# Kernel tuning notes

Measured on AMD Instinct MI355X. Metric: run time of the kernel, lower is better.

The kernel has to match this reference:

```python
import jax, jax.numpy as jnp
import numpy as np

B, D = 4096, 1024

def setup_inputs() -> dict:
    key = jax.random.key(0)
    k1, k2, k3 = jax.random.split(key, 3)
    # q, p are row-stochastic probability distributions (original calls q.log())
    q = jax.nn.softmax(jax.random.normal(k1, (B, D), dtype=jnp.float32), axis=-1)
    p = jax.nn.softmax(jax.random.normal(k2, (B, D), dtype=jnp.float32), axis=-1)
    # binary same-class indicator matrix
    labels_matrix = jax.random.randint(k3, (B, B), 0, 2).astype(jnp.float32)
    return {"q": q, "p": p, "labels_matrix": labels_matrix}

def reference(q, p, labels_matrix):
    d = q.shape[1]
    log_q = jnp.log(q)
    log_p = jnp.log(p)
    # torch kl_div(log_q, p) = p * (log p - log q); mean over feature dim -> [B]
    kl_div = jnp.mean(p * (log_p - log_q), axis=1)
    # pairwise kl_dis[i, j] = mean_d p[j,d] * (log p[j,d] - log q[i,d])
    # = (sum_d p[j] log p[j] - (log_q @ p^T)[i, j]) / D  -- single GEMM, no BxBxD tensor
    p_entropy_term = jnp.sum(p * log_p, axis=1)          # [B]
    cross = log_q @ p.T                                   # [B, B]
    kl_dis = (p_entropy_term[None, :] - cross) / d        # [B, B]
    # original detaches kl_dis via .cpu().numpy()
    kl_dis = jax.lax.stop_gradient(kl_dis)
    positive = kl_div + jnp.sum(kl_dis * labels_matrix, axis=1)
    negative = jnp.sum(kl_dis * (1.0 - labels_matrix), axis=1)
    return jnp.sum(positive / negative)
```

## Files before the change

kernel.cpp:

```cpp
#include <hip/hip_runtime.h>
#include <hip/hip_bf16.h>
#include <stdint.h>

#define BROWS 4096
#define DDIM  1024
#define LSTR  72

typedef float f32x4 __attribute__((ext_vector_type(4)));
#define PSCALE 64.0f
#define INV_PSCALE 0.015625f

__device__ __forceinline__ int pack4_fp8(float a, float b, float c, float d) {
    int w = __builtin_amdgcn_cvt_pk_fp8_f32(a, b, 0, false);
    w = __builtin_amdgcn_cvt_pk_fp8_f32(c, d, w, true);
    return w;
}

__global__ __launch_bounds__(256) void prep_kernel(
    const float* __restrict__ q, const float* __restrict__ p,
    const float* __restrict__ L,
    int* __restrict__ lq8, int* __restrict__ p8,
    uint64_t* __restrict__ Lb,
    float* __restrict__ e, float* __restrict__ kld,
    float* __restrict__ CS, float* __restrict__ CL, float* __restrict__ EL)
{
    const int row = blockIdx.x;
    const int t   = threadIdx.x;
    const int wv  = t >> 6, ln = t & 63;

    const float4* qv4 = (const float4*)(q + (size_t)row * DDIM);
    const float4* pv4 = (const float4*)(p + (size_t)row * DDIM);
    float4 qv = qv4[t];
    float4 pv = pv4[t];

    float lq0 = __logf(qv.x), lq1 = __logf(qv.y), lq2 = __logf(qv.z), lq3 = __logf(qv.w);
    float lp0 = __logf(pv.x), lp1 = __logf(pv.y), lp2 = __logf(pv.z), lp3 = __logf(pv.w);

    float esum = pv.x * lp0 + pv.y * lp1 + pv.z * lp2 + pv.w * lp3;
    float ksum = pv.x * (lp0 - lq0) + pv.y * (lp1 - lq1)
               + pv.z * (lp2 - lq2) + pv.w * (lp3 - lq3);

    lq8[row * 256 + t] = pack4_fp8(lq0, lq1, lq2, lq3);
    p8 [row * 256 + t] = pack4_fp8(pv.x * PSCALE, pv.y * PSCALE,
                                   pv.z * PSCALE, pv.w * PSCALE);

    const float* Lrow = L + (size_t)row * BROWS;
    #pragma unroll
    for (int c = 0; c < 16; c++) {
        float v = Lrow[c * 256 + t];
        unsigned long long m = __ballot(v != 0.0f);
        if (ln == 0) Lb[(size_t)row * 64 + c * 4 + wv] = m;
    }

    if (t == 0) { CS[row] = 0.f; CL[row] = 0.f; EL[row] = 0.f; }

    #pragma unroll
    for (int off = 32; off > 0; off >>= 1) {
        esum += __shfl_down(esum, off);
        ksum += __shfl_down(ksum, off);
    }
    __shared__ float se[4], sk[4];
    if (ln == 0) { se[wv] = esum; sk[wv] = ksum; }
    __syncthreads();
    if (t == 0) {
        e[row]   = se[0] + se[1] + se[2] + se[3];
        kld[row] = (sk[0] + sk[1] + sk[2] + sk[3]) * (1.0f / DDIM);
    }
}

__global__ __launch_bounds__(1024, 4) void gemm_epi_kernel(
    const uint8_t* __restrict__ A8,
    const uint8_t* __restrict__ B8,
    const uint64_t* __restrict__ Lb,
    const float*  __restrict__ e,
    float* __restrict__ CS, float* __restrict__ CL, float* __restrict__ EL)
{
    __shared__ __align__(16) uint8_t As[256 * LSTR];
    __shared__ __align__(16) uint8_t Bs[256 * LSTR];

    const int t    = threadIdx.x;
    const int i0   = blockIdx.y * 256;
    const int j0   = blockIdx.x * 256;
    const int wave = t >> 6;
    const int lane = t & 63;
    const int q4   = lane >> 4;
    const int ln   = lane & 15;
    const int wrow = wave & 3;
    const int wcol = wave >> 2;

    f32x4 acc[4][4];
    #pragma unroll
    for (int a = 0; a < 4; a++)
        #pragma unroll
        for (int b = 0; b < 4; b++)
            acc[a][b] = (f32x4){0.f, 0.f, 0.f, 0.f};

    const int srow = t >> 2;
    const int scol = (t & 3) * 16;
    const uint8_t* gA = A8 + (size_t)(i0 + srow) * DDIM + scol;
    const uint8_t* gB = B8 + (size_t)(j0 + srow) * DDIM + scol;
    const int loff = srow * LSTR + scol;

    int4 pfA[2], pfB[2];
    pfA[0] = *(const int4*)(gA);       pfB[0] = *(const int4*)(gB);
    pfA[1] = *(const int4*)(gA + 64);  pfB[1] = *(const int4*)(gB + 64);

    #pragma unroll 1
    for (int c = 0; c < DDIM / 64; ++c) {
        const int buf = c & 1;
        __syncthreads();
        *(int4*)(As + loff) = pfA[buf];
        *(int4*)(Bs + loff) = pfB[buf];
        __syncthreads();

        if (c + 2 < DDIM / 64) {
            pfA[buf] = *(const int4*)(gA + (c + 2) * 64);
            pfB[buf] = *(const int4*)(gB + (c + 2) * 64);
        }

        #pragma unroll
        for (int ks = 0; ks < 2; ks++) {
            long af[4], bfv[4];
            #pragma unroll
            for (int mi = 0; mi < 4; mi++)
                af[mi] = *(const long*)(As + (wrow * 64 + mi * 16 + ln) * LSTR
                                           + ks * 32 + q4 * 8);
            #pragma unroll
            for (int ni = 0; ni < 4; ni++)
                bfv[ni] = *(const long*)(Bs + (wcol * 64 + ni * 16 + ln) * LSTR
                                            + ks * 32 + q4 * 8);
            #pragma unroll
            for (int mi = 0; mi < 4; mi++)
                #pragma unroll
                for (int ni = 0; ni < 4; ni++)
                    acc[mi][ni] = __builtin_amdgcn_mfma_f32_16x16x32_fp8_fp8(
                        af[mi], bfv[ni], acc[mi][ni], 0, 0, 0);
        }
    }

    const int i_base = i0 + wrow * 64;
    const int j_base = j0 + wcol * 64;

    float e_j[4];
    #pragma unroll
    for (int ni = 0; ni < 4; ni++) e_j[ni] = e[j_base + ni * 16 + ln];

    #pragma unroll
    for (int mi = 0; mi < 4; mi++) {
        #pragma unroll
        for (int r = 0; r < 4; r++) {
            const int i = i_base + mi * 16 + q4 * 4 + r;
            const uint64_t m  = Lb[(size_t)i * 64 + (j_base >> 6)];
            const uint64_t ms = m >> ln;
            float cs = 0.f, cl = 0.f, el = 0.f;
            #pragma unroll
            for (int ni = 0; ni < 4; ni++) {
                float c = acc[mi][ni][r];
                cs += c;
                if ((ms >> (ni * 16)) & 1ull) { cl += c; el += e_j[ni]; }
            }
            #pragma unroll
            for (int s = 1; s < 16; s <<= 1) {
                cs += __shfl_xor(cs, s);
                cl += __shfl_xor(cl, s);
                el += __shfl_xor(el, s);
            }
            if (ln == 0) {
                atomicAdd(&CS[i], cs * INV_PSCALE);
                atomicAdd(&CL[i], cl * INV_PSCALE);
                atomicAdd(&EL[i], el);
            }
        }
    }
}

__global__ __launch_bounds__(1024) void final_kernel(
    const float* __restrict__ e, const float* __restrict__ kld,
    const float* __restrict__ CS, const float* __restrict__ CL,
    const float* __restrict__ EL, float* __restrict__ out)
{
    __shared__ float sred[16];
    __shared__ float sEtot;
    const int t = threadIdx.x;
    const int wv = t >> 6, ln = t & 63;

    float s = 0.f;
    for (int j = t; j < BROWS; j += 1024) s += e[j];
    #pragma unroll
    for (int off = 32; off > 0; off >>= 1) s += __shfl_down(s, off);
    if (ln == 0) sred[wv] = s;
    __syncthreads();
    if (t == 0) {
        float a = 0.f;
        #pragma unroll
        for (int k = 0; k < 16; k++) a += sred[k];
        sEtot = a;
    }
    __syncthreads();
    const float Etot = sEtot;
    const float invD = 1.0f / DDIM;

    float rs = 0.f;
    for (int i = t; i < BROWS; i += 1024) {
        float el = EL[i], cl = CL[i], cs = CS[i];
        float pos = kld[i] + (el - cl) * invD;
        float neg = (Etot - el - cs + cl) * invD;
        rs += pos / neg;
    }
    __syncthreads();
    #pragma unroll
    for (int off = 32; off > 0; off >>= 1) rs += __shfl_down(rs, off);
    if (ln == 0) sred[wv] = rs;
    __syncthreads();
    if (t == 0) {
        float a = 0.f;
        #pragma unroll
        for (int k = 0; k < 16; k++) a += sred[k];
        out[0] = a;
    }
}

extern "C" void kernel_launch(void* const* d_in, const int* in_sizes, int n_in,
                              void* d_out, int out_size, void* d_ws, size_t ws_size,
                              hipStream_t stream)
{
    const float* q = (const float*)d_in[0];
    const float* p = (const float*)d_in[1];
    const float* L = (const float*)d_in[2];
    float* out = (float*)d_out;

    char* ws = (char*)d_ws;
    int*  lq8 = (int*)ws;
    int*  p8  = (int*)(ws + (size_t)BROWS * DDIM);
    float* e  = (float*)(ws + (size_t)BROWS * DDIM * 2);
    float* kld = e + BROWS;
    float* CS  = kld + BROWS;
    float* CL  = CS + BROWS;
    float* EL  = CL + BROWS;
    uint64_t* Lb = (uint64_t*)(EL + BROWS);

    prep_kernel<<<BROWS, 256, 0, stream>>>(q, p, L, lq8, p8, Lb, e, kld, CS, CL, EL);

    dim3 grid(BROWS / 256, BROWS / 256);
    gemm_epi_kernel<<<grid, 1024, 0, stream>>>(
        (const uint8_t*)lq8, (const uint8_t*)p8, Lb, e, CS, CL, EL);

    final_kernel<<<1, 1024, 0, stream>>>(e, kld, CS, CL, EL, out);
}
```

Baseline: 203.5 us.

## Permute fp8 K layout for 128-bit LDS fragment loads and shrink GEMM tile

The prep kernel now writes the fp8 operands in a permuted K order. This lets each lane fetch both k-sub-steps' fragments with one 16-byte LDS read instead of two 8-byte reads, and the LDS row stride is padded to 80 bytes to match. The GEMM tile shrinks from 256x256 with 1024 threads to 256x128 with 512 threads, doubling the grid, which may improve occupancy and balance at the cost of more B-side reloads and more atomics. The final reduction kernel is also trimmed to 256 threads.

```diff
diff --git a/kernel.cpp b/kernel.cpp
--- a/kernel.cpp
+++ b/kernel.cpp
@@ -4,9 +4,10 @@
 
 #define BROWS 4096
 #define DDIM  1024
-#define LSTR  72
+#define LSTR  80
 
 typedef float f32x4 __attribute__((ext_vector_type(4)));
+typedef long  lx2   __attribute__((ext_vector_type(2)));
 #define PSCALE 64.0f
 #define INV_PSCALE 0.015625f
 
@@ -40,9 +41,16 @@
     float ksum = pv.x * (lp0 - lq0) + pv.y * (lp1 - lq1)
                + pv.z * (lp2 - lq2) + pv.w * (lp3 - lq3);
 
-    lq8[row * 256 + t] = pack4_fp8(lq0, lq1, lq2, lq3);
-    p8 [row * 256 + t] = pack4_fp8(pv.x * PSCALE, pv.y * PSCALE,
-                                   pv.z * PSCALE, pv.w * PSCALE);
+    const int c0    = t * 4;
+    const int chunk = c0 >> 6;
+    const int c6    = c0 & 63;
+    const int ksb   = (c6 >> 5) & 1;
+    const int q4v   = (c6 >> 3) & 3;
+    const int rr    = c6 & 7;
+    const int newc  = chunk * 64 + q4v * 16 + ksb * 8 + rr;
+    const int idx   = (row * DDIM + newc) >> 2;
+    lq8[idx] = pack4_fp8(lq0, lq1, lq2, lq3);
+    p8 [idx] = pack4_fp8(pv.x * PSCALE, pv.y * PSCALE, pv.z * PSCALE, pv.w * PSCALE);
 
     const float* Lrow = L + (size_t)row * BROWS;
     #pragma unroll
@@ -68,7 +76,7 @@
     }
 }
 
-__global__ __launch_bounds__(1024, 4) void gemm_epi_kernel(
+__global__ __launch_bounds__(512, 4) void gemm_epi_kernel(
     const uint8_t* __restrict__ A8,
     const uint8_t* __restrict__ B8,
     const uint64_t* __restrict__ Lb,
@@ -76,11 +84,11 @@
     float* __restrict__ CS, float* __restrict__ CL, float* __restrict__ EL)
 {
     __shared__ __align__(16) uint8_t As[256 * LSTR];
-    __shared__ __align__(16) uint8_t Bs[256 * LSTR];
+    __shared__ __align__(16) uint8_t Bs[128 * LSTR];
 
     const int t    = threadIdx.x;
     const int i0   = blockIdx.y * 256;
-    const int j0   = blockIdx.x * 256;
+    const int j0   = blockIdx.x * 128;
     const int wave = t >> 6;
     const int lane = t & 63;
     const int q4   = lane >> 4;
@@ -95,47 +103,56 @@
         for (int b = 0; b < 4; b++)
             acc[a][b] = (f32x4){0.f, 0.f, 0.f, 0.f};
 
-    const int srow = t >> 2;
-    const int scol = (t & 3) * 16;
-    const uint8_t* gA = A8 + (size_t)(i0 + srow) * DDIM + scol;
-    const uint8_t* gB = B8 + (size_t)(j0 + srow) * DDIM + scol;
-    const int loff = srow * LSTR + scol;
-
-    int4 pfA[2], pfB[2];
-    pfA[0] = *(const int4*)(gA);       pfB[0] = *(const int4*)(gB);
-    pfA[1] = *(const int4*)(gA + 64);  pfB[1] = *(const int4*)(gB + 64);
+    const int uA0 = t, uA1 = t + 512, uB0 = t;
+    const uint8_t* gA0 = A8 + (size_t)(i0 + (uA0 >> 2)) * DDIM + (uA0 & 3) * 16;
+    const uint8_t* gA1 = A8 + (size_t)(i0 + (uA1 >> 2)) * DDIM + (uA1 & 3) * 16;
+    const uint8_t* gB0 = B8 + (size_t)(j0 + (uB0 >> 2)) * DDIM + (uB0 & 3) * 16;
+    const int lA0 = (uA0 >> 2) * LSTR + (uA0 & 3) * 16;
+    const int lA1 = (uA1 >> 2) * LSTR + (uA1 & 3) * 16;
+    const int lB0 = (uB0 >> 2) * LSTR + (uB0 & 3) * 16;
+
+    int4 pfA0[2], pfA1[2], pfB0[2];
+    pfA0[0] = *(const int4*)(gA0);      pfA1[0] = *(const int4*)(gA1);
+    pfB0[0] = *(const int4*)(gB0);
+    pfA0[1] = *(const int4*)(gA0 + 64); pfA1[1] = *(const int4*)(gA1 + 64);
+    pfB0[1] = *(const int4*)(gB0 + 64);
 
     #pragma unroll 1
     for (int c = 0; c < DDIM / 64; ++c) {
         const int buf = c & 1;
         __syncthreads();
-        *(int4*)(As + loff) = pfA[buf];
-        *(int4*)(Bs + loff) = pfB[buf];
+        *(int4*)(As + lA0) = pfA0[buf];
+        *(int4*)(As + lA1) = pfA1[buf];
+        *(int4*)(Bs + lB0) = pfB0[buf];
         __syncthreads();
 
         if (c + 2 < DDIM / 64) {
-            pfA[buf] = *(const int4*)(gA + (c + 2) * 64);
-            pfB[buf] = *(const int4*)(gB + (c + 2) * 64);
+            const int k = (c + 2) * 64;
+            pfA0[buf] = *(const int4*)(gA0 + k);
+            pfA1[buf] = *(const int4*)(gA1 + k);
+            pfB0[buf] = *(const int4*)(gB0 + k);
         }
 
-        #pragma unroll
-        for (int ks = 0; ks < 2; ks++) {
-            long af[4], bfv[4];
-            #pragma unroll
-            for (int mi = 0; mi < 4; mi++)
-                af[mi] = *(const long*)(As + (wrow * 64 + mi * 16 + ln) * LSTR
-                                           + ks * 32 + q4 * 8);
+        lx2 a2[4], b2[4];
+        #pragma unroll
+        for (int mi = 0; mi < 4; mi++)
+            a2[mi] = *(const lx2*)(As + (wrow * 64 + mi * 16 + ln) * LSTR + q4 * 16);
+        #pragma unroll
+        for (int ni = 0; ni < 4; ni++)
+            b2[ni] = *(const lx2*)(Bs + (wcol * 64 + ni * 16 + ln) * LSTR + q4 * 16);
+
+        #pragma unroll
+        for (int mi = 0; mi < 4; mi++)
             #pragma unroll
             for (int ni = 0; ni < 4; ni++)
-                bfv[ni] = *(const long*)(Bs + (wcol * 64 + ni * 16 + ln) * LSTR
-                                            + ks * 32 + q4 * 8);
-            #pragma unroll
-            for (int mi = 0; mi < 4; mi++)
-                #pragma unroll
-                for (int ni = 0; ni < 4; ni++)
-                    acc[mi][ni] = __builtin_amdgcn_mfma_f32_16x16x32_fp8_fp8(
-                        af[mi], bfv[ni], acc[mi][ni], 0, 0, 0);
-        }
+                acc[mi][ni] = __builtin_amdgcn_mfma_f32_16x16x32_fp8_fp8(
+                    a2[mi].x, b2[ni].x, acc[mi][ni], 0, 0, 0);
+        #pragma unroll
+        for (int mi = 0; mi < 4; mi++)
+            #pragma unroll
+            for (int ni = 0; ni < 4; ni++)
+                acc[mi][ni] = __builtin_amdgcn_mfma_f32_16x16x32_fp8_fp8(
+                    a2[mi].y, b2[ni].y, acc[mi][ni], 0, 0, 0);
     }
 
     const int i_base = i0 + wrow * 64;
@@ -174,34 +191,29 @@
     }
 }
 
-__global__ __launch_bounds__(1024) void final_kernel(
+__global__ __launch_bounds__(256) void final_kernel(
     const float* __restrict__ e, const float* __restrict__ kld,
     const float* __restrict__ CS, const float* __restrict__ CL,
     const float* __restrict__ EL, float* __restrict__ out)
 {
-    __shared__ float sred[16];
+    __shared__ float sred[4];
     __shared__ float sEtot;
     const int t = threadIdx.x;
     const int wv = t >> 6, ln = t & 63;
 
     float s = 0.f;
-    for (int j = t; j < BROWS; j += 1024) s += e[j];
+    for (int j = t; j < BROWS; j += 256) s += e[j];
     #pragma unroll
     for (int off = 32; off > 0; off >>= 1) s += __shfl_down(s, off);
     if (ln == 0) sred[wv] = s;
     __syncthreads();
-    if (t == 0) {
-        float a = 0.f;
-        #pragma unroll
-        for (int k = 0; k < 16; k++) a += sred[k];
-        sEtot = a;
-    }
+    if (t == 0) sEtot = sred[0] + sred[1] + sred[2] + sred[3];
     __syncthreads();
     const float Etot = sEtot;
     const float invD = 1.0f / DDIM;
 
     float rs = 0.f;
-    for (int i = t; i < BROWS; i += 1024) {
+    for (int i = t; i < BROWS; i += 256) {
         float el = EL[i], cl = CL[i], cs = CS[i];
         float pos = kld[i] + (el - cl) * invD;
         float neg = (Etot - el - cs + cl) * invD;
@@ -212,12 +224,7 @@
     for (int off = 32; off > 0; off >>= 1) rs += __shfl_down(rs, off);
     if (ln == 0) sred[wv] = rs;
     __syncthreads();
-    if (t == 0) {
-        float a = 0.f;
-        #pragma unroll
-        for (int k = 0; k < 16; k++) a += sred[k];
-        out[0] = a;
-    }
+    if (t == 0) out[0] = sred[0] + sred[1] + sred[2] + sred[3];
 }
 
 extern "C" void kernel_launch(void* const* d_in, const int* in_sizes, int n_in,
@@ -241,9 +248,9 @@
 
     prep_kernel<<<BROWS, 256, 0, stream>>>(q, p, L, lq8, p8, Lb, e, kld, CS, CL, EL);
 
-    dim3 grid(BROWS / 256, BROWS / 256);
-    gemm_epi_kernel<<<grid, 1024, 0, stream>>>(
+    dim3 grid(BROWS / 128, BROWS / 256);
+    gemm_epi_kernel<<<grid, 512, 0, stream>>>(
         (const uint8_t*)lq8, (const uint8_t*)p8, Lb, e, CS, CL, EL);
 
-    final_kernel<<<1, 1024, 0, stream>>>(e, kld, CS, CL, EL, out);
-}
+    final_kernel<<<1, 256, 0, stream>>>(e, kld, CS, CL, EL, out);
+}
```

After: 220.6 us. +8.4%, slower.
